# Optimization experiments

Measured on AMD Instinct MI355X. Metric: run time of the kernel, lower is better.

Reference implementation:

```python
import jax, jax.numpy as jnp
import numpy as np

L, B, H = 4096, 32, 1024

def setup_inputs() -> dict:
    key = jax.random.key(0)
    k1, k2 = jax.random.split(key)
    hidden = jax.random.normal(k1, (H, B), dtype=jnp.float32)
    encoder_outputs = jax.random.normal(k2, (L, B, H), dtype=jnp.float32)
    return {"hidden": hidden, "encoder_outputs": encoder_outputs}

def reference(hidden, encoder_outputs):
    # 'dot' score: energies[b, l] = hidden[:, b] . encoder_outputs[l, b, :]
    energies = jnp.einsum('hb,lbh->bl', hidden, encoder_outputs)  # [B, L]
    attn = jax.nn.softmax(energies, axis=1)                        # [B, L]
    return attn[:, None, :]                                        # [B, 1, L]
```

## Files before the change

### kernel.cpp

```cpp
#include <hip/hip_runtime.h>
#include <math.h>

#define L_DIM 4096
#define B_DIM 32
#define H_DIM 1024

__global__ void transpose_hidden_k(const float* __restrict__ hidden,
                                   float* __restrict__ hT) {
    int tid = blockIdx.x * blockDim.x + threadIdx.x;
    int h = tid / B_DIM;
    int b = tid % B_DIM;
    hT[b * H_DIM + h] = hidden[tid];
}

__device__ __forceinline__ float dot4(float4 a, float4 b) {
    return a.x * b.x + a.y * b.y + a.z * b.z + a.w * b.w;
}

__global__ __launch_bounds__(256) void energies_k(const float* __restrict__ hT,
                                                  const float* __restrict__ enc,
                                                  float* __restrict__ out) {
    const int bid  = blockIdx.x;
    const int b    = bid & 31;
    const int cg   = bid >> 5;
    const int t    = threadIdx.x;
    const int wave = t >> 6;
    const int lane = t & 63;

    const float4* hp = (const float4*)(hT + (size_t)b * H_DIM);
    const float4 h0 = hp[lane      ];
    const float4 h1 = hp[lane +  64];
    const float4 h2 = hp[lane + 128];
    const float4 h3 = hp[lane + 192];

    const int l0 = cg * 64 + wave * 16;
    const size_t rowstride = (size_t)B_DIM * H_DIM;
    const float* rp = enc + (size_t)l0 * rowstride + (size_t)b * H_DIM;
    float* orow = out + (size_t)b * L_DIM + l0;

    for (int i = 0; i < 16; i += 4) {
        const float4* r0 = (const float4*)(rp + (size_t)(i + 0) * rowstride);
        const float4* r1 = (const float4*)(rp + (size_t)(i + 1) * rowstride);
        const float4* r2 = (const float4*)(rp + (size_t)(i + 2) * rowstride);
        const float4* r3 = (const float4*)(rp + (size_t)(i + 3) * rowstride);

        float4 a00 = r0[lane], a01 = r0[lane + 64], a02 = r0[lane + 128], a03 = r0[lane + 192];
        float4 a10 = r1[lane], a11 = r1[lane + 64], a12 = r1[lane + 128], a13 = r1[lane + 192];
        float4 a20 = r2[lane], a21 = r2[lane + 64], a22 = r2[lane + 128], a23 = r2[lane + 192];
        float4 a30 = r3[lane], a31 = r3[lane + 64], a32 = r3[lane + 128], a33 = r3[lane + 192];

        float acc0 = dot4(a00, h0) + dot4(a01, h1) + dot4(a02, h2) + dot4(a03, h3);
        float acc1 = dot4(a10, h0) + dot4(a11, h1) + dot4(a12, h2) + dot4(a13, h3);
        float acc2 = dot4(a20, h0) + dot4(a21, h1) + dot4(a22, h2) + dot4(a23, h3);
        float acc3 = dot4(a30, h0) + dot4(a31, h1) + dot4(a32, h2) + dot4(a33, h3);

#pragma unroll
        for (int off = 32; off > 0; off >>= 1) {
            acc0 += __shfl_down(acc0, off, 64);
            acc1 += __shfl_down(acc1, off, 64);
            acc2 += __shfl_down(acc2, off, 64);
            acc3 += __shfl_down(acc3, off, 64);
        }
        if (lane == 0) {
            float4 o = make_float4(acc0, acc1, acc2, acc3);
            *(float4*)(orow + i) = o;
        }
    }
}

__global__ __launch_bounds__(1024) void softmax_k(float* __restrict__ out) {
    __shared__ float red[16];
    const int b = blockIdx.x;
    float* row = out + (size_t)b * L_DIM;
    const int t = threadIdx.x;
    const int lane = t & 63;
    const int wave = t >> 6;

    float vals[4];
    float m = -INFINITY;
#pragma unroll
    for (int k = 0; k < 4; ++k) {
        vals[k] = row[t + k * 1024];
        m = fmaxf(m, vals[k]);
    }
#pragma unroll
    for (int off = 32; off > 0; off >>= 1)
        m = fmaxf(m, __shfl_down(m, off, 64));
    if (lane == 0) red[wave] = m;
    __syncthreads();
    float mm = red[0];
#pragma unroll
    for (int w = 1; w < 16; ++w) mm = fmaxf(mm, red[w]);
    __syncthreads();

    float s = 0.f;
#pragma unroll
    for (int k = 0; k < 4; ++k) {
        vals[k] = expf(vals[k] - mm);
        s += vals[k];
    }
#pragma unroll
    for (int off = 32; off > 0; off >>= 1)
        s += __shfl_down(s, off, 64);
    if (lane == 0) red[wave] = s;
    __syncthreads();
    float ss = 0.f;
#pragma unroll
    for (int w = 0; w < 16; ++w) ss += red[w];

    const float inv = 1.0f / ss;
#pragma unroll
    for (int k = 0; k < 4; ++k)
        row[t + k * 1024] = vals[k] * inv;
}

extern "C" void kernel_launch(void* const* d_in, const int* in_sizes, int n_in,
                              void* d_out, int out_size, void* d_ws, size_t ws_size,
                              hipStream_t stream) {
    const float* hidden = (const float*)d_in[0];
    const float* enc    = (const float*)d_in[1];
    float* out = (float*)d_out;
    float* hT  = (float*)d_ws;

    transpose_hidden_k<<<(H_DIM * B_DIM) / 256, 256, 0, stream>>>(hidden, hT);
    energies_k<<<B_DIM * 64, 256, 0, stream>>>(hT, enc, out);
    softmax_k<<<B_DIM, 1024, 0, stream>>>(out);
}
```

Measured before the change: 691.9 us.

## Fuse hidden transpose into energies kernel and quadruple grid with fewer rows per wave

Removes the separate transpose kernel: each energies block gathers its batch column of hidden into shared memory with strided global loads. The grid grows from 2048 to 8192 blocks, and each wave now handles 4 rows instead of 16 with no loop. The intent is to save a launch and expose more parallelism and loads in flight for the bandwidth-bound 512MB read. In exchange, every block repeats the strided gather of hidden (uncoalesced, 4x more blocks) and pays a barrier.

Result: faster. 670.5 us (-3.1%).

```diff
diff --git a/kernel.cpp b/kernel.cpp
--- a/kernel.cpp
+++ b/kernel.cpp
@@ -5,21 +5,14 @@
 #define B_DIM 32
 #define H_DIM 1024
 
-__global__ void transpose_hidden_k(const float* __restrict__ hidden,
-                                   float* __restrict__ hT) {
-    int tid = blockIdx.x * blockDim.x + threadIdx.x;
-    int h = tid / B_DIM;
-    int b = tid % B_DIM;
-    hT[b * H_DIM + h] = hidden[tid];
-}
-
 __device__ __forceinline__ float dot4(float4 a, float4 b) {
     return a.x * b.x + a.y * b.y + a.z * b.z + a.w * b.w;
 }
 
-__global__ __launch_bounds__(256) void energies_k(const float* __restrict__ hT,
+__global__ __launch_bounds__(256) void energies_k(const float* __restrict__ hidden,
                                                   const float* __restrict__ enc,
                                                   float* __restrict__ out) {
+    __shared__ float sh[H_DIM];
     const int bid  = blockIdx.x;
     const int b    = bid & 31;
     const int cg   = bid >> 5;
@@ -27,44 +20,43 @@
     const int wave = t >> 6;
     const int lane = t & 63;
 
-    const float4* hp = (const float4*)(hT + (size_t)b * H_DIM);
-    const float4 h0 = hp[lane      ];
-    const float4 h1 = hp[lane +  64];
-    const float4 h2 = hp[lane + 128];
-    const float4 h3 = hp[lane + 192];
+#pragma unroll
+    for (int k = 0; k < 4; ++k)
+        sh[t + k * 256] = hidden[(t + k * 256) * B_DIM + b];
+    __syncthreads();
 
-    const int l0 = cg * 64 + wave * 16;
+    const int l0 = cg * 16 + wave * 4;
     const size_t rowstride = (size_t)B_DIM * H_DIM;
     const float* rp = enc + (size_t)l0 * rowstride + (size_t)b * H_DIM;
-    float* orow = out + (size_t)b * L_DIM + l0;
+    const float4* sp = (const float4*)sh;
 
-    for (int i = 0; i < 16; i += 4) {
-        const float4* r0 = (const float4*)(rp + (size_t)(i + 0) * rowstride);
-        const float4* r1 = (const float4*)(rp + (size_t)(i + 1) * rowstride);
-        const float4* r2 = (const float4*)(rp + (size_t)(i + 2) * rowstride);
-        const float4* r3 = (const float4*)(rp + (size_t)(i + 3) * rowstride);
+    const float4* r0 = (const float4*)(rp);
+    const float4* r1 = (const float4*)(rp + rowstride);
+    const float4* r2 = (const float4*)(rp + 2 * rowstride);
+    const float4* r3 = (const float4*)(rp + 3 * rowstride);
 
-        float4 a00 = r0[lane], a01 = r0[lane + 64], a02 = r0[lane + 128], a03 = r0[lane + 192];
-        float4 a10 = r1[lane], a11 = r1[lane + 64], a12 = r1[lane + 128], a13 = r1[lane + 192];
-        float4 a20 = r2[lane], a21 = r2[lane + 64], a22 = r2[lane + 128], a23 = r2[lane + 192];
-        float4 a30 = r3[lane], a31 = r3[lane + 64], a32 = r3[lane + 128], a33 = r3[lane + 192];
+    float4 a00 = r0[lane], a01 = r0[lane + 64], a02 = r0[lane + 128], a03 = r0[lane + 192];
+    float4 a10 = r1[lane], a11 = r1[lane + 64], a12 = r1[lane + 128], a13 = r1[lane + 192];
+    float4 a20 = r2[lane], a21 = r2[lane + 64], a22 = r2[lane + 128], a23 = r2[lane + 192];
+    float4 a30 = r3[lane], a31 = r3[lane + 64], a32 = r3[lane + 128], a33 = r3[lane + 192];
 
-        float acc0 = dot4(a00, h0) + dot4(a01, h1) + dot4(a02, h2) + dot4(a03, h3);
-        float acc1 = dot4(a10, h0) + dot4(a11, h1) + dot4(a12, h2) + dot4(a13, h3);
-        float acc2 = dot4(a20, h0) + dot4(a21, h1) + dot4(a22, h2) + dot4(a23, h3);
-        float acc3 = dot4(a30, h0) + dot4(a31, h1) + dot4(a32, h2) + dot4(a33, h3);
+    float4 h0 = sp[lane], h1 = sp[lane + 64], h2 = sp[lane + 128], h3 = sp[lane + 192];
+
+    float acc0 = dot4(a00, h0) + dot4(a01, h1) + dot4(a02, h2) + dot4(a03, h3);
+    float acc1 = dot4(a10, h0) + dot4(a11, h1) + dot4(a12, h2) + dot4(a13, h3);
+    float acc2 = dot4(a20, h0) + dot4(a21, h1) + dot4(a22, h2) + dot4(a23, h3);
+    float acc3 = dot4(a30, h0) + dot4(a31, h1) + dot4(a32, h2) + dot4(a33, h3);
 
 #pragma unroll
-        for (int off = 32; off > 0; off >>= 1) {
-            acc0 += __shfl_down(acc0, off, 64);
-            acc1 += __shfl_down(acc1, off, 64);
-            acc2 += __shfl_down(acc2, off, 64);
-            acc3 += __shfl_down(acc3, off, 64);
-        }
-        if (lane == 0) {
-            float4 o = make_float4(acc0, acc1, acc2, acc3);
-            *(float4*)(orow + i) = o;
-        }
+    for (int off = 32; off > 0; off >>= 1) {
+        acc0 += __shfl_down(acc0, off, 64);
+        acc1 += __shfl_down(acc1, off, 64);
+        acc2 += __shfl_down(acc2, off, 64);
+        acc3 += __shfl_down(acc3, off, 64);
+    }
+    if (lane == 0) {
+        float4 o = make_float4(acc0, acc1, acc2, acc3);
+        *(float4*)(out + (size_t)b * L_DIM + l0) = o;
     }
 }
 
@@ -120,9 +112,8 @@
     const float* hidden = (const float*)d_in[0];
     const float* enc    = (const float*)d_in[1];
     float* out = (float*)d_out;
-    float* hT  = (float*)d_ws;
+    (void)d_ws; (void)ws_size;
 
-    transpose_hidden_k<<<(H_DIM * B_DIM) / 256, 256, 0, stream>>>(hidden, hT);
-    energies_k<<<B_DIM * 64, 256, 0, stream>>>(hT, enc, out);
+    energies_k<<<B_DIM * 256, 256, 0, stream>>>(hidden, enc, out);
     softmax_k<<<B_DIM, 1024, 0, stream>>>(out);
 }
```
